# Optimization experiments

Hardware: AMD Instinct MI355X
Metric: run time of the kernel (lower is better)

Reference implementation:

```python
import jax, jax.numpy as jnp
import numpy as np

H = 16      # query heads
KV = 8      # kv heads
D = 128     # head_dim
HID = 2048  # hidden_size
T = 2048    # tokens
EPS = 1e-6
THETA = 1000000.0


def setup_inputs() -> dict:
    key = jax.random.key(0)
    ks = jax.random.split(key, 4)
    return {
        "hidden_states": jax.random.normal(ks[0], (T, HID), jnp.float32),
        "positions": jnp.arange(T, dtype=jnp.int32),
        "qkv_w": jax.random.normal(ks[1], (H * D + 2 * KV * D, HID), jnp.float32) * 0.02,
        "o_w": jax.random.normal(ks[2], (HID, H * D), jnp.float32) * 0.02,
        "q_norm_w": jnp.ones((D,), jnp.float32),
        "k_norm_w": jnp.ones((D,), jnp.float32),
    }


def _rmsnorm(x, w):
    # x: [T, heads, D]; normalize over last dim
    var = jnp.mean(x * x, axis=-1, keepdims=True)
    return x * jax.lax.rsqrt(var + EPS) * w


def _rope(x, positions):
    # neox-style rotate-half; x: [T, heads, D]
    half = D // 2
    inv_freq = 1.0 / (THETA ** (jnp.arange(0, half, dtype=jnp.float32) / half * 1.0))
    inv_freq = 1.0 / (THETA ** (jnp.arange(0, D, 2, dtype=jnp.float32) / D))
    ang = positions.astype(jnp.float32)[:, None] * inv_freq  # [T, D/2]
    cos = jnp.cos(ang)[:, None, :]
    sin = jnp.sin(ang)[:, None, :]
    x1, x2 = x[..., :half], x[..., half:]
    return jnp.concatenate([x1 * cos - x2 * sin, x2 * cos + x1 * sin], axis=-1)


def reference(hidden_states, positions, qkv_w, o_w, q_norm_w, k_norm_w):
    scale = D ** -0.5
    qkv = hidden_states @ qkv_w.T  # [T, H*D + 2*KV*D]
    q = qkv[:, : H * D].reshape(T, H, D)
    k = qkv[:, H * D : H * D + KV * D].reshape(T, KV, D)
    v = qkv[:, H * D + KV * D :].reshape(T, KV, D)

    q = _rope(_rmsnorm(q, q_norm_w), positions)
    k = _rope(_rmsnorm(k, k_norm_w), positions)

    # GQA: repeat kv heads to match query heads
    rep = H // KV
    k = jnp.repeat(k, rep, axis=1)  # [T, H, D]
    v = jnp.repeat(v, rep, axis=1)

    scores = jnp.einsum("thd,shd->hts", q, k) * scale  # [H, T, T]
    causal = positions[:, None] >= positions[None, :]  # [T, T]
    scores = jnp.where(causal[None, :, :], scores, jnp.float32(-1e30))
    p = jax.nn.softmax(scores, axis=-1)
    o = jnp.einsum("hts,shd->thd", p, v).reshape(T, H * D)
    return o @ o_w.T  # [T, HID]
```

## Files before the change

kernel.cpp:

```cpp
#include <hip/hip_runtime.h>
#include <math.h>

#define T_TOK 2048
#define HID 2048
#define NH 16
#define NKV 8
#define HD 128
#define QKV_N 4096
#define EPS 1e-6f

typedef unsigned short u16;
typedef unsigned int   u32;
typedef __attribute__((ext_vector_type(8))) u16   u16x8;
typedef __attribute__((ext_vector_type(8))) short short8;
typedef __attribute__((ext_vector_type(4))) float floatx4;
typedef __attribute__((ext_vector_type(16))) float f32x16;
typedef __attribute__((ext_vector_type(4))) u32   u32x4;

__device__ __forceinline__ u16 f2bf(float x) {
    u32 u = __float_as_uint(x);
    u = (u + 0x7fffu + ((u >> 16) & 1u)) >> 16;
    return (u16)u;
}
__device__ __forceinline__ float bf2f(u16 h) {
    return __uint_as_float(((u32)h) << 16);
}
__device__ __forceinline__ u32 cvtpk_bf16(float lo, float hi) {
    u32 r;
    asm("v_cvt_pk_bf16_f32 %0, %1, %2" : "=v"(r) : "v"(lo), "v"(hi));
    return r;
}

__device__ __forceinline__ void cvt8(const float* __restrict__ in,
                                     u16* __restrict__ out, size_t i)
{
    float4 a = *(const float4*)(in + i);
    float4 b = *(const float4*)(in + i + 4);
    u16x8 o;
    o[0] = f2bf(a.x); o[1] = f2bf(a.y); o[2] = f2bf(a.z); o[3] = f2bf(a.w);
    o[4] = f2bf(b.x); o[5] = f2bf(b.y); o[6] = f2bf(b.z); o[7] = f2bf(b.w);
    *(u16x8*)(out + i) = o;
}

__global__ __launch_bounds__(256) void cvt_pair(
    const float* __restrict__ ina, u16* __restrict__ outa,
    const float* __restrict__ inb, u16* __restrict__ outb)
{
    const int bid = blockIdx.x;
    if (bid < 2048) cvt8(ina, outa, ((size_t)bid * 256 + threadIdx.x) * 8);
    else            cvt8(inb, outb, ((size_t)(bid - 2048) * 256 + threadIdx.x) * 8);
}

#define GBM 256
#define GBN 128
#define GBK 64
#define BUFSH 24576

#define WAITV6 asm volatile("s_waitcnt vmcnt(6)" ::: "memory")
#define WAITV0 asm volatile("s_waitcnt vmcnt(0)" ::: "memory")
#define LGKM0  asm volatile("s_waitcnt lgkmcnt(0)" ::: "memory")
#define BARR   asm volatile("s_barrier" ::: "memory")
#define SB     __builtin_amdgcn_sched_barrier(0)

#define STAGEU(i, tt, dstb) \
    __builtin_amdgcn_global_load_lds( \
        (const __attribute__((address_space(1))) u32*)(gsrc[i] + (size_t)(tt)*GBK), \
        (__attribute__((address_space(3))) u32*)((dstb) + loff[i]), 16, 0, 0)

#define RD_A(dst, srcb, f) do { \
    dst[0] = *(const short8*)((srcb) + arow + (f)*1024 + achunk0); \
    dst[1] = *(const short8*)((srcb) + arow + (f)*1024 + achunk1); } while (0)

#define RD_B(dst, srcb) do { \
    _Pragma("unroll") \
    for (int j_ = 0; j_ < 4; ++j_) { \
        dst[j_][0] = *(const short8*)((srcb) + 16384 + brow + j_*1024 + achunk0); \
        dst[j_][1] = *(const short8*)((srcb) + 16384 + brow + j_*1024 + achunk1); } } while (0)

#define MM(f, aa, bb) do { \
    __builtin_amdgcn_s_setprio(1); \
    _Pragma("unroll") \
    for (int j_ = 0; j_ < 4; ++j_) { \
        acc[f][j_] = __builtin_amdgcn_mfma_f32_16x16x32_bf16(aa[0], bb[j_][0], acc[f][j_], 0, 0, 0); \
        acc[f][j_] = __builtin_amdgcn_mfma_f32_16x16x32_bf16(aa[1], bb[j_][1], acc[f][j_], 0, 0, 0); } \
    __builtin_amdgcn_s_setprio(0); } while (0)

#define TILE(t, CURB, NXTB, THDB, BBC, BBN) do { \
    const bool st_ = (t) + 2 < nt; \
    if (st_) { STAGEU(0, (t)+2, THDB); STAGEU(1, (t)+2, THDB); } \
    RD_A(aP1, CURB, 1); SB; \
    MM(0, aP0, BBC); SB; \
    if (st_) { STAGEU(2, (t)+2, THDB); STAGEU(3, (t)+2, THDB); } \
    RD_A(aP0, CURB, 2); SB; \
    MM(1, aP1, BBC); SB; \
    if (st_) { STAGEU(4, (t)+2, THDB); STAGEU(5, (t)+2, THDB); } \
    RD_A(aP1, CURB, 3); SB; \
    MM(2, aP0, BBC); \
    if ((t) + 1 < nt) { \
        if (st_) { WAITV6; } else { WAITV0; } \
        LGKM0; BARR; SB; \
        RD_B(BBN, NXTB); RD_A(aP0, NXTB, 0); \
    } \
    SB; \
    MM(3, aP1, BBC); SB; \
} while (0)

template<bool OUT_BF16>
__global__ __launch_bounds__(512, 2) void gemm_bt_8p(
    const u16* __restrict__ A, const u16* __restrict__ B,
    void* __restrict__ Cv, int K, int lda, int ldb, int ldc)
{
    extern __shared__ short lds[];
    const int tid = threadIdx.x;
    const int w  = tid >> 6;
    const int l  = tid & 63;
    const int m0 = blockIdx.y * GBM;
    const int n0 = blockIdx.x * GBN;
    const int mr = (w >> 1) * 64;
    const int nc = (w & 1) * 64;
    const int cc = l & 15;
    const int q4 = l >> 4;

    const int lr = l >> 3;
    const int gchunk = ((l & 7) ^ (lr & 7)) * 8;
    const u16* gsrc[6]; int loff[6];
    #pragma unroll
    for (int i = 0; i < 6; ++i) {
        const int u = w * 6 + i;
        if (u < 32) {
            gsrc[i] = A + (size_t)(m0 + u*8 + lr) * lda + gchunk;
            loff[i] = u * 512;
        } else {
            const int v = u - 32;
            gsrc[i] = B + (size_t)(n0 + v*8 + lr) * ldb + gchunk;
            loff[i] = 16384 + v * 512;
        }
    }

    const int achunk0 = ((q4)     ^ (cc & 7)) * 8;
    const int achunk1 = ((4 + q4) ^ (cc & 7)) * 8;
    const int arow = (mr + cc) * 64;
    const int brow = (nc + cc) * 64;

    floatx4 acc[4][4];
    #pragma unroll
    for (int f = 0; f < 4; ++f)
        #pragma unroll
        for (int j = 0; j < 4; ++j) acc[f][j] = (floatx4){0.f, 0.f, 0.f, 0.f};

    short8 aP0[2], aP1[2], bbE[4][2], bbO[4][2];
    short* b0 = lds;
    short* b1 = lds + BUFSH;
    short* b2 = lds + 2 * BUFSH;
    const int nt = K >> 6;

    #pragma unroll
    for (int i = 0; i < 6; ++i) STAGEU(i, 0, b0);
    #pragma unroll
    for (int i = 0; i < 6; ++i) STAGEU(i, 1, b1);
    WAITV6; BARR; SB;
    RD_B(bbE, b0); RD_A(aP0, b0, 0);

    short *CURB = b0, *NXTB = b1, *THDB = b2;
    for (int t = 0; t < nt; t += 2) {
        TILE(t, CURB, NXTB, THDB, bbE, bbO);
        { short* tmp = CURB; CURB = NXTB; NXTB = THDB; THDB = tmp; }
        TILE(t + 1, CURB, NXTB, THDB, bbO, bbE);
        { short* tmp = CURB; CURB = NXTB; NXTB = THDB; THDB = tmp; }
    }

    const int r0 = q4 * 4;
    #pragma unroll
    for (int f = 0; f < 4; ++f)
        #pragma unroll
        for (int j = 0; j < 4; ++j)
            #pragma unroll
            for (int r = 0; r < 4; ++r) {
                const int row = m0 + mr + f*16 + r0 + r;
                const int col = n0 + nc + j*16 + cc;
                if (OUT_BF16)
                    ((u16*)Cv)[(size_t)row * ldc + col] = f2bf(acc[f][j][r]);
                else
                    ((float*)Cv)[(size_t)row * ldc + col] = acc[f][j][r];
            }
}

__global__ __launch_bounds__(256) void prep(
    u16* __restrict__ qkv, const int* __restrict__ positions,
    const float* __restrict__ qw, const float* __restrict__ kw,
    u16* __restrict__ Kp, u16* __restrict__ Vtp)
{
    const int bid = blockIdx.x;
    const int tile = bid & 31, kvh = bid >> 5;
    const int tid = threadIdx.x;
    const int w = tid >> 6, l = tid & 63;
    const int t0 = tile * 64;

    const float qw0 = qw[2*l], qw1 = qw[2*l+1];
    const float kw0 = kw[2*l], kw1 = kw[2*l+1];
    const int   i0  = (2*l) & 63;
    const float if0 = exp2f(-(float)i0     * 0.311430758895690f);
    const float if1 = exp2f(-(float)(i0+1) * 0.311430758895690f);

    for (int rr = w; rr < 64; rr += 4) {
        const int t = t0 + rr;
        const int pos = positions[t];
        const float a0 = (float)pos * if0;
        const float a1 = (float)pos * if1;
        const float s0 = sinf(a0), c0 = cosf(a0);
        const float s1 = sinf(a1), c1 = cosf(a1);

        #pragma unroll
        for (int pass = 0; pass < 3; ++pass) {
            const int off = (pass < 2) ? (2*kvh + pass)*HD : NH*HD + kvh*HD;
            const float w0 = (pass < 2) ? qw0 : kw0;
            const float w1 = (pass < 2) ? qw1 : kw1;
            u16* p = qkv + (size_t)t*QKV_N + off;

            const u32 pk = *(const u32*)(p + 2*l);
            const float x0 = bf2f((u16)pk), x1 = bf2f((u16)(pk >> 16));
            float ss = x0*x0 + x1*x1;
            #pragma unroll
            for (int x = 1; x < 64; x <<= 1) ss += __shfl_xor(ss, x);
            const float rs = rsqrtf(ss * (1.0f/128.0f) + EPS);
            const float xn0 = x0 * rs * w0, xn1 = x1 * rs * w1;
            const float px0 = __shfl_xor(xn0, 32);
            const float px1 = __shfl_xor(xn1, 32);

            float o0, o1;
            if (l < 32) { o0 = xn0*c0 - px0*s0; o1 = xn1*c1 - px1*s1; }
            else        { o0 = xn0*c0 + px0*s0; o1 = xn1*c1 + px1*s1; }
            const u32 outpk = (u32)f2bf(o0) | ((u32)f2bf(o1) << 16);

            if (pass < 2) {
                *(u32*)(p + 2*l) = outpk;
            } else {
                const int ch = l >> 2;
                u16* dst = Kp + ((size_t)(kvh*32 + tile)*64 + rr)*128
                              + (ch ^ (rr & 15))*8 + (l & 3)*2;
                *(u32*)dst = outpk;
            }
        }
    }

    __shared__ u16 tl[64][136];
    {
        const int t  = tid >> 2;
        const int c0 = (tid & 3) * 32;
        const u16* src = qkv + (size_t)(t0 + t)*QKV_N + NH*HD + NKV*HD + kvh*HD + c0;
        #pragma unroll
        for (int p2 = 0; p2 < 4; ++p2)
            *(u16x8*)(&tl[t][c0 + p2*8]) = *(const u16x8*)(src + p2*8);
    }
    __syncthreads();
    {
        u16* dstb = Vtp + (size_t)(kvh*32 + tile) * 128 * 64;
        #pragma unroll
        for (int i = 0; i < 4; ++i) {
            const int id = tid*4 + i;
            const int d = id >> 3;
            const int o = id & 7;
            const int sb = (o ^ (d & 7)) * 8;
            u16x8 v;
            #pragma unroll
            for (int j = 0; j < 8; ++j) v[j] = tl[sb + j][d];
            *(u16x8*)(dstb + d*64 + o*8) = v;
        }
    }
}

__global__ __launch_bounds__(256, 2) void attn_mfma32(
    const u16* __restrict__ qkv, const u16* __restrict__ Kp,
    const u16* __restrict__ Vtp,
    u16* __restrict__ P0, u16* __restrict__ P1,
    u16* __restrict__ P2, u16* __restrict__ P3,
    float2* __restrict__ ml)
{
    const int id   = blockIdx.x;
    const int kvh  = id & 7;
    const int u    = id >> 3;
    const int b5   = u >> 5;
    const int r5   = u & 31;
    const int hp   = r5 & 1;
    const int part = (r5 >> 1) & 3;
    const int q3   = r5 >> 3;
    const int qt   = b5 ? 7 - q3 : q3;
    const int h    = kvh*2 + hp;
    const int t0q  = qt * 256;

    const int tid = threadIdx.x;
    const int w   = tid >> 6;
    const int l   = tid & 63;
    const int q31 = l & 31;
    const int hi  = l >> 5;

    __shared__ short Ks[2][8192];
    __shared__ short Vts[2][8192];

    short8 qf[2][8];
    #pragma unroll
    for (int qg = 0; qg < 2; ++qg) {
        const u16* qrow = qkv + (size_t)(t0q + w*64 + qg*32 + q31) * QKV_N + h*HD;
        #pragma unroll
        for (int ks = 0; ks < 8; ++ks)
            qf[qg][ks] = *(const short8*)(qrow + ks*16 + hi*8);
    }

    float m_run[2] = {-3.0e38f, -3.0e38f}, l_run[2] = {0.f, 0.f};
    f32x16 accO[2][4];
    #pragma unroll
    for (int qg = 0; qg < 2; ++qg)
        #pragma unroll
        for (int nd = 0; nd < 4; ++nd)
            #pragma unroll
            for (int r = 0; r < 16; ++r) accO[qg][nd][r] = 0.f;

    const float Cs = 0.12751744f;

    const int tlo = part * (qt + 1);
    const int thi = tlo + (qt + 1);

    auto issue = [&](int tile, int buf) {
        const size_t tb = (size_t)(kvh*32 + tile) * 8192;
        const u16* g = ((w < 2) ? Kp : Vtp) + tb + (w & 1)*4096 + l*8;
        short* p = ((w < 2) ? Ks[buf] : Vts[buf]) + (w & 1)*4096 + l*8;
        #pragma unroll
        for (int i = 0; i < 8; ++i)
            __builtin_amdgcn_global_load_lds(
                (const __attribute__((address_space(1))) u32*)(g + i*512),
                (__attribute__((address_space(3))) u32*)(p + i*512), 16, 0, 0);
    };

    issue(tlo, 0);
    int cur = 0;

    for (int tt = tlo; tt < thi; ++tt) {
        __syncthreads();
        if (tt + 1 < thi) issue(tt + 1, cur ^ 1);

        const short* Kc = Ks[cur];
        const short* Vc = Vts[cur];

        #pragma unroll
        for (int sub = 0; sub < 2; ++sub) {
            f32x16 accS[2];
            #pragma unroll
            for (int r = 0; r < 16; ++r) { accS[0][r] = 0.f; accS[1][r] = 0.f; }

            __builtin_amdgcn_s_setprio(1);
            #pragma unroll
            for (int ks = 0; ks < 8; ++ks) {
                short8 a = *(const short8*)(Kc + (sub*32 + q31)*128
                                            + ((2*ks + hi) ^ (q31 & 15))*8);
                accS[0] = __builtin_amdgcn_mfma_f32_32x32x16_bf16(a, qf[0][ks], accS[0], 0, 0, 0);
                accS[1] = __builtin_amdgcn_mfma_f32_32x32x16_bf16(a, qf[1][ks], accS[1], 0, 0, 0);
            }
            __builtin_amdgcn_s_setprio(0);

            if (tt >= 4*qt) {
                const int kvb0 = tt*64 + sub*32 + (hi<<2);
                #pragma unroll
                for (int qg = 0; qg < 2; ++qg) {
                    const int qg_g = t0q + w*64 + qg*32 + q31;
                    #pragma unroll
                    for (int r = 0; r < 16; ++r) {
                        const int kvg = kvb0 + (r&3) + 8*(r>>2);
                        if (kvg > qg_g) accS[qg][r] = -1.0e30f;
                    }
                }
            }

            #pragma unroll
            for (int qg = 0; qg < 2; ++qg) {
                float mx = accS[qg][0];
                #pragma unroll
                for (int r = 1; r < 16; ++r) mx = fmaxf(mx, accS[qg][r]);
                mx = fmaxf(mx, __shfl_xor(mx, 32));

                if (__any(mx > m_run[qg] + 11.76f)) {
                    const float m_new = fmaxf(m_run[qg], mx);
                    const float alpha = exp2f((m_run[qg] - m_new) * Cs);
                    l_run[qg] *= alpha;
                    m_run[qg] = m_new;
                    #pragma unroll
                    for (int r = 0; r < 16; ++r) {
                        const float ar = __shfl(alpha, ((r&3) + 8*(r>>2)) + (hi<<2));
                        accO[qg][0][r] *= ar; accO[qg][1][r] *= ar;
                        accO[qg][2][r] *= ar; accO[qg][3][r] *= ar;
                    }
                }
                const float mb = m_run[qg] * Cs;
                float lsum = 0.f;
                #pragma unroll
                for (int r = 0; r < 16; ++r) {
                    const float e = exp2f(accS[qg][r]*Cs - mb);
                    accS[qg][r] = e;
                    lsum += e;
                }
                lsum += __shfl_xor(lsum, 32);
                l_run[qg] += lsum;
            }

            __builtin_amdgcn_s_setprio(1);
            #pragma unroll
            for (int ks2 = 0; ks2 < 2; ++ks2) {
                const int R = ks2 * 8;
                short8 aP[2];
                #pragma unroll
                for (int qg = 0; qg < 2; ++qg) {
                    u32 x0 = cvtpk_bf16(accS[qg][R+0], accS[qg][R+1]);
                    u32 x1 = cvtpk_bf16(accS[qg][R+2], accS[qg][R+3]);
                    u32 x2 = cvtpk_bf16(accS[qg][R+4], accS[qg][R+5]);
                    u32 x3 = cvtpk_bf16(accS[qg][R+6], accS[qg][R+7]);
                    asm("v_permlane32_swap_b32 %0, %1" : "+v"(x0), "+v"(x2));
                    asm("v_permlane32_swap_b32 %0, %1" : "+v"(x1), "+v"(x3));
                    u32x4 aw; aw.x = x0; aw.y = x1; aw.z = x2; aw.w = x3;
                    aP[qg] = __builtin_bit_cast(short8, aw);
                }
                const int ksg = sub*2 + ks2;
                #pragma unroll
                for (int nd = 0; nd < 4; ++nd) {
                    short8 bv = *(const short8*)(Vc + (nd*32 + q31)*64
                                                 + ((2*ksg + hi) ^ (q31 & 7))*8);
                    accO[0][nd] = __builtin_amdgcn_mfma_f32_32x32x16_bf16(aP[0], bv, accO[0][nd], 0, 0, 0);
                    accO[1][nd] = __builtin_amdgcn_mfma_f32_32x32x16_bf16(aP[1], bv, accO[1][nd], 0, 0, 0);
                }
            }
            __builtin_amdgcn_s_setprio(0);
        }
        cur ^= 1;
    }

    u16* Op = (part == 0) ? P0 : (part == 1) ? P1 : (part == 2) ? P2 : P3;
    const size_t hb = (size_t)h * T_TOK;
    #pragma unroll
    for (int qg = 0; qg < 2; ++qg) {
        #pragma unroll
        for (int r = 0; r < 16; ++r) {
            const int qr = (r&3) + 8*(r>>2) + (hi<<2);
            u16* op = Op + (hb + t0q + w*64 + qg*32 + qr) * HD;
            op[q31]      = f2bf(accO[qg][0][r]);
            op[32 + q31] = f2bf(accO[qg][1][r]);
            op[64 + q31] = f2bf(accO[qg][2][r]);
            op[96 + q31] = f2bf(accO[qg][3][r]);
        }
        if (l < 32)
            ml[(size_t)part*NH*T_TOK + hb + t0q + w*64 + qg*32 + l]
                = make_float2(m_run[qg], l_run[qg]);
    }
}

__global__ __launch_bounds__(256) void combine4_cvt(
    const u16* __restrict__ P0, const u16* __restrict__ P1,
    const u16* __restrict__ P2, const u16* __restrict__ P3,
    const float2* __restrict__ ml, u16* __restrict__ qkv,
    const float* __restrict__ ow, u16* __restrict__ owbf)
{
    const int bid = blockIdx.x;
    if (bid >= 2048) {
        cvt8(ow, owbf, ((size_t)(bid - 2048) * 256 + threadIdx.x) * 8);
        return;
    }
    const int idx = bid * 256 + threadIdx.x;
    const int c16 = idx & 15;
    const int t   = (idx >> 4) & (T_TOK - 1);
    const int h   = idx >> 15;
    const size_t base = (size_t)h * T_TOK + t;
    const size_t NT = (size_t)NH * T_TOK;
    const float2 a = ml[base];
    const float2 b = ml[base + NT];
    const float2 c = ml[base + 2*NT];
    const float2 d = ml[base + 3*NT];
    const float Cs = 0.12751744f;
    const float mM = fmaxf(fmaxf(a.x, b.x), fmaxf(c.x, d.x));
    const float wA = exp2f((a.x - mM) * Cs);
    const float wB = exp2f((b.x - mM) * Cs);
    const float wC = exp2f((c.x - mM) * Cs);
    const float wD = exp2f((d.x - mM) * Cs);
    const float inv = 1.0f / (wA*a.y + wB*b.y + wC*c.y + wD*d.y);
    const u16x8 A = *(const u16x8*)(P0 + base * HD + c16*8);
    const u16x8 B = *(const u16x8*)(P1 + base * HD + c16*8);
    const u16x8 C = *(const u16x8*)(P2 + base * HD + c16*8);
    const u16x8 D = *(const u16x8*)(P3 + base * HD + c16*8);
    u16x8 o;
    #pragma unroll
    for (int j = 0; j < 8; ++j)
        o[j] = f2bf((wA*bf2f(A[j]) + wB*bf2f(B[j]) + wC*bf2f(C[j]) + wD*bf2f(D[j])) * inv);
    *(u16x8*)(qkv + (size_t)t * QKV_N + h * HD + c16*8) = o;
}

extern "C" void kernel_launch(void* const* d_in, const int* in_sizes, int n_in,
                              void* d_out, int out_size, void* d_ws, size_t ws_size,
                              hipStream_t stream)
{
    const float* hidden    = (const float*)d_in[0];
    const int*   positions = (const int*)  d_in[1];
    const float* qkv_w     = (const float*)d_in[2];
    const float* o_w       = (const float*)d_in[3];
    const float* q_norm_w  = (const float*)d_in[4];
    const float* k_norm_w  = (const float*)d_in[5];
    float* out = (float*)d_out;

    u16* qkvbf = (u16*)d_ws;
    u16* wbf   = qkvbf + (size_t)T_TOK * QKV_N;
    u16* abf   = wbf   + (size_t)QKV_N * HID;
    u16* kpb   = abf   + (size_t)T_TOK * HID;
    u16* vpb   = kpb   + (size_t)NKV * T_TOK * HD;

    u16* P0 = wbf;
    u16* P1 = wbf + (size_t)NH * T_TOK * HD;
    u16* P2 = abf;
    u16* P3 = (u16*)out;
    float2* mlp = (float2*)((u16*)out + (size_t)NH * T_TOK * HD);

    static bool s_attr = false;
    if (!s_attr) {
        (void)hipFuncSetAttribute(
            reinterpret_cast<const void*>(&gemm_bt_8p<true>),
            hipFuncAttributeMaxDynamicSharedMemorySize, 147456);
        (void)hipFuncSetAttribute(
            reinterpret_cast<const void*>(&gemm_bt_8p<false>),
            hipFuncAttributeMaxDynamicSharedMemorySize, 147456);
        s_attr = true;
    }

    cvt_pair<<<6144, 256, 0, stream>>>(hidden, abf, qkv_w, wbf);

    gemm_bt_8p<true><<<dim3(QKV_N/GBN, T_TOK/GBM), 512, 147456, stream>>>(
        abf, wbf, qkvbf, HID, HID, HID, QKV_N);

    prep<<<256, 256, 0, stream>>>(qkvbf, positions, q_norm_w, k_norm_w, kpb, vpb);

    attn_mfma32<<<512, 256, 0, stream>>>(qkvbf, kpb, vpb, P0, P1, P2, P3, mlp);

    combine4_cvt<<<4096, 256, 0, stream>>>(P0, P1, P2, P3, mlp, qkvbf, o_w, kpb);

    gemm_bt_8p<false><<<dim3(HID/GBN, T_TOK/GBM), 512, 147456, stream>>>(
        qkvbf, kpb, out, HID, QKV_N, HID, HID);
}
```

Before: 268.6 us.

## Halve attention query and KV tiles, double grid and occupancy

The attention kernel now works on 128-row query tiles (32 rows per wave) and 32-token KV tiles instead of 256/64. The grid doubles to 1024 blocks and launch bounds allow 4 blocks per CU. The V-transpose layout in prep and the LDS swizzle change to match 32-token tiles. This aims to improve occupancy and load balance across the causal work. In exchange, each K/V tile loaded into LDS is reused by fewer query rows, and there are twice as many barriers per unit of work.

```diff
diff --git a/kernel.cpp b/kernel.cpp
--- a/kernel.cpp
+++ b/kernel.cpp
@@ -254,22 +254,21 @@
     }
     __syncthreads();
     {
-        u16* dstb = Vtp + (size_t)(kvh*32 + tile) * 128 * 64;
+        u16* dstb = Vtp + (size_t)(kvh*64 + tile*2) * 4096;
         #pragma unroll
         for (int i = 0; i < 4; ++i) {
             const int id = tid*4 + i;
             const int d = id >> 3;
             const int o = id & 7;
-            const int sb = (o ^ (d & 7)) * 8;
             u16x8 v;
             #pragma unroll
-            for (int j = 0; j < 8; ++j) v[j] = tl[sb + j][d];
-            *(u16x8*)(dstb + d*64 + o*8) = v;
-        }
-    }
-}
-
-__global__ __launch_bounds__(256, 2) void attn_mfma32(
+            for (int j = 0; j < 8; ++j) v[j] = tl[o*8 + j][d];
+            *(u16x8*)(dstb + (o >> 2)*4096 + d*32 + (((o & 3) ^ (d & 3)))*8) = v;
+        }
+    }
+}
+
+__global__ __launch_bounds__(256, 4) void attn_mfma32(
     const u16* __restrict__ qkv, const u16* __restrict__ Kp,
     const u16* __restrict__ Vtp,
     u16* __restrict__ P0, u16* __restrict__ P1,
@@ -279,14 +278,14 @@
     const int id   = blockIdx.x;
     const int kvh  = id & 7;
     const int u    = id >> 3;
-    const int b5   = u >> 5;
-    const int r5   = u & 31;
-    const int hp   = r5 & 1;
-    const int part = (r5 >> 1) & 3;
-    const int q3   = r5 >> 3;
-    const int qt   = b5 ? 7 - q3 : q3;
+    const int hp   = u & 1;
+    const int part = (u >> 1) & 3;
+    const int q4b  = u >> 3;
+    const int g    = q4b & 3;
+    const int s4   = q4b >> 2;
+    const int qt   = (s4 & 1) ? (2*g + (s4 >> 1)) : ((15 - (s4 >> 1)) - 2*g);
     const int h    = kvh*2 + hp;
-    const int t0q  = qt * 256;
+    const int t0q  = qt * 128;
 
     const int tid = threadIdx.x;
     const int w   = tid >> 6;
@@ -294,40 +293,37 @@
     const int q31 = l & 31;
     const int hi  = l >> 5;
 
-    __shared__ short Ks[2][8192];
-    __shared__ short Vts[2][8192];
-
-    short8 qf[2][8];
-    #pragma unroll
-    for (int qg = 0; qg < 2; ++qg) {
-        const u16* qrow = qkv + (size_t)(t0q + w*64 + qg*32 + q31) * QKV_N + h*HD;
+    __shared__ short Ks[2][4096];
+    __shared__ short Vts[2][4096];
+
+    short8 qf[8];
+    {
+        const u16* qrow = qkv + (size_t)(t0q + w*32 + q31) * QKV_N + h*HD;
         #pragma unroll
         for (int ks = 0; ks < 8; ++ks)
-            qf[qg][ks] = *(const short8*)(qrow + ks*16 + hi*8);
-    }
-
-    float m_run[2] = {-3.0e38f, -3.0e38f}, l_run[2] = {0.f, 0.f};
-    f32x16 accO[2][4];
-    #pragma unroll
-    for (int qg = 0; qg < 2; ++qg)
-        #pragma unroll
-        for (int nd = 0; nd < 4; ++nd)
-            #pragma unroll
-            for (int r = 0; r < 16; ++r) accO[qg][nd][r] = 0.f;
+            qf[ks] = *(const short8*)(qrow + ks*16 + hi*8);
+    }
+
+    float m_run = -3.0e38f, l_run = 0.f;
+    f32x16 accO[4];
+    #pragma unroll
+    for (int nd = 0; nd < 4; ++nd)
+        #pragma unroll
+        for (int r = 0; r < 16; ++r) accO[nd][r] = 0.f;
 
     const float Cs = 0.12751744f;
 
     const int tlo = part * (qt + 1);
     const int thi = tlo + (qt + 1);
 
-    auto issue = [&](int tile, int buf) {
-        const size_t tb = (size_t)(kvh*32 + tile) * 8192;
-        const u16* g = ((w < 2) ? Kp : Vtp) + tb + (w & 1)*4096 + l*8;
-        short* p = ((w < 2) ? Ks[buf] : Vts[buf]) + (w & 1)*4096 + l*8;
-        #pragma unroll
-        for (int i = 0; i < 8; ++i)
+    auto issue = [&](int t32, int buf) {
+        const size_t tb = (size_t)(kvh*64 + t32) * 4096;
+        const u16* g2 = ((w < 2) ? Kp : Vtp) + tb + (w & 1)*2048 + l*8;
+        short* p = ((w < 2) ? Ks[buf] : Vts[buf]) + (w & 1)*2048 + l*8;
+        #pragma unroll
+        for (int i = 0; i < 4; ++i)
             __builtin_amdgcn_global_load_lds(
-                (const __attribute__((address_space(1))) u32*)(g + i*512),
+                (const __attribute__((address_space(1))) u32*)(g2 + i*512),
                 (__attribute__((address_space(3))) u32*)(p + i*512), 16, 0, 0);
     };
 
@@ -341,113 +337,99 @@
         const short* Kc = Ks[cur];
         const short* Vc = Vts[cur];
 
-        #pragma unroll
-        for (int sub = 0; sub < 2; ++sub) {
-            f32x16 accS[2];
+        f32x16 accS;
+        #pragma unroll
+        for (int r = 0; r < 16; ++r) accS[r] = 0.f;
+
+        __builtin_amdgcn_s_setprio(1);
+        #pragma unroll
+        for (int ks = 0; ks < 8; ++ks) {
+            short8 a = *(const short8*)(Kc + q31*128 + ((2*ks + hi) ^ (q31 & 15))*8);
+            accS = __builtin_amdgcn_mfma_f32_32x32x16_bf16(a, qf[ks], accS, 0, 0, 0);
+        }
+        __builtin_amdgcn_s_setprio(0);
+
+        if (tt >= 4*qt) {
+            const int kvb0 = tt*32 + (hi << 2);
+            const int qg_g = t0q + w*32 + q31;
             #pragma unroll
-            for (int r = 0; r < 16; ++r) { accS[0][r] = 0.f; accS[1][r] = 0.f; }
-
-            __builtin_amdgcn_s_setprio(1);
+            for (int r = 0; r < 16; ++r) {
+                const int kvg = kvb0 + (r&3) + 8*(r>>2);
+                if (kvg > qg_g) accS[r] = -1.0e30f;
+            }
+        }
+
+        float mx = accS[0];
+        #pragma unroll
+        for (int r = 1; r < 16; ++r) mx = fmaxf(mx, accS[r]);
+        mx = fmaxf(mx, __shfl_xor(mx, 32));
+
+        if (__any(mx > m_run + 11.76f)) {
+            const float m_new = fmaxf(m_run, mx);
+            const float alpha = exp2f((m_run - m_new) * Cs);
+            l_run *= alpha;
+            m_run = m_new;
             #pragma unroll
-            for (int ks = 0; ks < 8; ++ks) {
-                short8 a = *(const short8*)(Kc + (sub*32 + q31)*128
-                                            + ((2*ks + hi) ^ (q31 & 15))*8);
-                accS[0] = __builtin_amdgcn_mfma_f32_32x32x16_bf16(a, qf[0][ks], accS[0], 0, 0, 0);
-                accS[1] = __builtin_amdgcn_mfma_f32_32x32x16_bf16(a, qf[1][ks], accS[1], 0, 0, 0);
+            for (int r = 0; r < 16; ++r) {
+                const float ar = __shfl(alpha, ((r&3) + 8*(r>>2)) + (hi<<2));
+                accO[0][r] *= ar; accO[1][r] *= ar;
+                accO[2][r] *= ar; accO[3][r] *= ar;
             }
-            __builtin_amdgcn_s_setprio(0);
-
-            if (tt >= 4*qt) {
-                const int kvb0 = tt*64 + sub*32 + (hi<<2);
-                #pragma unroll
-                for (int qg = 0; qg < 2; ++qg) {
-                    const int qg_g = t0q + w*64 + qg*32 + q31;
-                    #pragma unroll
-                    for (int r = 0; r < 16; ++r) {
-                        const int kvg = kvb0 + (r&3) + 8*(r>>2);
-                        if (kvg > qg_g) accS[qg][r] = -1.0e30f;
-                    }
-                }
+        }
+        const float mb = m_run * Cs;
+        float lsum = 0.f;
+        #pragma unroll
+        for (int r = 0; r < 16; ++r) {
+            const float e = exp2f(accS[r]*Cs - mb);
+            accS[r] = e;
+            lsum += e;
+        }
+        lsum += __shfl_xor(lsum, 32);
+        l_run += lsum;
+
+        short8 aP[2];
+        #pragma unroll
+        for (int ks2 = 0; ks2 < 2; ++ks2) {
+            const int R = ks2 * 8;
+            u32 x0 = cvtpk_bf16(accS[R+0], accS[R+1]);
+            u32 x1 = cvtpk_bf16(accS[R+2], accS[R+3]);
+            u32 x2 = cvtpk_bf16(accS[R+4], accS[R+5]);
+            u32 x3 = cvtpk_bf16(accS[R+6], accS[R+7]);
+            asm("v_permlane32_swap_b32 %0, %1" : "+v"(x0), "+v"(x2));
+            asm("v_permlane32_swap_b32 %0, %1" : "+v"(x1), "+v"(x3));
+            u32x4 aw; aw.x = x0; aw.y = x1; aw.z = x2; aw.w = x3;
+            aP[ks2] = __builtin_bit_cast(short8, aw);
+        }
+
+        __builtin_amdgcn_s_setprio(1);
+        #pragma unroll
+        for (int ks2 = 0; ks2 < 2; ++ks2) {
+            #pragma unroll
+            for (int nd = 0; nd < 4; ++nd) {
+                short8 bv = *(const short8*)(Vc + (nd*32 + q31)*32
+                                             + ((ks2*2 + hi) ^ (q31 & 3))*8);
+                accO[nd] = __builtin_amdgcn_mfma_f32_32x32x16_bf16(aP[ks2], bv, accO[nd], 0, 0, 0);
             }
-
-            #pragma unroll
-            for (int qg = 0; qg < 2; ++qg) {
-                float mx = accS[qg][0];
-                #pragma unroll
-                for (int r = 1; r < 16; ++r) mx = fmaxf(mx, accS[qg][r]);
-                mx = fmaxf(mx, __shfl_xor(mx, 32));
-
-                if (__any(mx > m_run[qg] + 11.76f)) {
-                    const float m_new = fmaxf(m_run[qg], mx);
-                    const float alpha = exp2f((m_run[qg] - m_new) * Cs);
-                    l_run[qg] *= alpha;
-                    m_run[qg] = m_new;
-                    #pragma unroll
-                    for (int r = 0; r < 16; ++r) {
-                        const float ar = __shfl(alpha, ((r&3) + 8*(r>>2)) + (hi<<2));
-                        accO[qg][0][r] *= ar; accO[qg][1][r] *= ar;
-                        accO[qg][2][r] *= ar; accO[qg][3][r] *= ar;
-                    }
-                }
-                const float mb = m_run[qg] * Cs;
-                float lsum = 0.f;
-                #pragma unroll
-                for (int r = 0; r < 16; ++r) {
-                    const float e = exp2f(accS[qg][r]*Cs - mb);
-                    accS[qg][r] = e;
-                    lsum += e;
-                }
-                lsum += __shfl_xor(lsum, 32);
-                l_run[qg] += lsum;
-            }
-
-            __builtin_amdgcn_s_setprio(1);
-            #pragma unroll
-            for (int ks2 = 0; ks2 < 2; ++ks2) {
-                const int R = ks2 * 8;
-                short8 aP[2];
-                #pragma unroll
-                for (int qg = 0; qg < 2; ++qg) {
-                    u32 x0 = cvtpk_bf16(accS[qg][R+0], accS[qg][R+1]);
-                    u32 x1 = cvtpk_bf16(accS[qg][R+2], accS[qg][R+3]);
-                    u32 x2 = cvtpk_bf16(accS[qg][R+4], accS[qg][R+5]);
-                    u32 x3 = cvtpk_bf16(accS[qg][R+6], accS[qg][R+7]);
-                    asm("v_permlane32_swap_b32 %0, %1" : "+v"(x0), "+v"(x2));
-                    asm("v_permlane32_swap_b32 %0, %1" : "+v"(x1), "+v"(x3));
-                    u32x4 aw; aw.x = x0; aw.y = x1; aw.z = x2; aw.w = x3;
-                    aP[qg] = __builtin_bit_cast(short8, aw);
-                }
-                const int ksg = sub*2 + ks2;
-                #pragma unroll
-                for (int nd = 0; nd < 4; ++nd) {
-                    short8 bv = *(const short8*)(Vc + (nd*32 + q31)*64
-                                                 + ((2*ksg + hi) ^ (q31 & 7))*8);
-                    accO[0][nd] = __builtin_amdgcn_mfma_f32_32x32x16_bf16(aP[0], bv, accO[0][nd], 0, 0, 0);
-                    accO[1][nd] = __builtin_amdgcn_mfma_f32_32x32x16_bf16(aP[1], bv, accO[1][nd], 0, 0, 0);
-                }
-            }
-            __builtin_amdgcn_s_setprio(0);
-        }
+        }
+        __builtin_amdgcn_s_setprio(0);
+
         cur ^= 1;
     }
 
     u16* Op = (part == 0) ? P0 : (part == 1) ? P1 : (part == 2) ? P2 : P3;
     const size_t hb = (size_t)h * T_TOK;
     #pragma unroll
-    for (int qg = 0; qg < 2; ++qg) {
-        #pragma unroll
-        for (int r = 0; r < 16; ++r) {
-            const int qr = (r&3) + 8*(r>>2) + (hi<<2);
-            u16* op = Op + (hb + t0q + w*64 + qg*32 + qr) * HD;
-            op[q31]      = f2bf(accO[qg][0][r]);
-            op[32 + q31] = f2bf(accO[qg][1][r]);
-            op[64 + q31] = f2bf(accO[qg][2][r]);
-            op[96 + q31] = f2bf(accO[qg][3][r]);
-        }
-        if (l < 32)
-            ml[(size_t)part*NH*T_TOK + hb + t0q + w*64 + qg*32 + l]
-                = make_float2(m_run[qg], l_run[qg]);
-    }
+    for (int r = 0; r < 16; ++r) {
+        const int qr = (r&3) + 8*(r>>2) + (hi<<2);
+        u16* op = Op + (hb + t0q + w*32 + qr) * HD;
+        op[q31]      = f2bf(accO[0][r]);
+        op[32 + q31] = f2bf(accO[1][r]);
+        op[64 + q31] = f2bf(accO[2][r]);
+        op[96 + q31] = f2bf(accO[3][r]);
+    }
+    if (l < 32)
+        ml[(size_t)part*NH*T_TOK + hb + t0q + w*32 + l]
+            = make_float2(m_run, l_run);
 }
 
 __global__ __launch_bounds__(256) void combine4_cvt(
@@ -531,7 +513,7 @@
 
     prep<<<256, 256, 0, stream>>>(qkvbf, positions, q_norm_w, k_norm_w, kpb, vpb);
 
-    attn_mfma32<<<512, 256, 0, stream>>>(qkvbf, kpb, vpb, P0, P1, P2, P3, mlp);
+    attn_mfma32<<<1024, 256, 0, stream>>>(qkvbf, kpb, vpb, P0, P1, P2, P3, mlp);
 
     combine4_cvt<<<4096, 256, 0, stream>>>(P0, P1, P2, P3, mlp, qkvbf, o_w, kpb);
 
```

Result: no change. 272.0 us (+1.3%).

## Split-K the output projection and rebalance attention blocks across both heads of a KV group

Applied to the files above, without the earlier changes.

The output projection GEMM gets a split-K mode: a grid z-dimension of 2 gives each half of K its own block and partial output, and a new elementwise kernel adds the two fp32 partials. This doubles the number of blocks for the small 2048x2048 GEMM, which otherwise launches only 128 blocks, to raise CU occupancy, at the cost of an extra read/write pass over the output. Separately, the attention kernel now gives each block 128 query rows for both query heads sharing one KV head, instead of 256 rows for one head. KV tiles are split evenly over the 4 partitions, and the causal mask is shared across both heads. This reuses each loaded K/V tile for two heads and balances causal work, with slight changes to setprio placement.

```diff
diff --git a/kernel.cpp b/kernel.cpp
--- a/kernel.cpp
+++ b/kernel.cpp
@@ -49,6 +49,20 @@
     const int bid = blockIdx.x;
     if (bid < 2048) cvt8(ina, outa, ((size_t)bid * 256 + threadIdx.x) * 8);
     else            cvt8(inb, outb, ((size_t)(bid - 2048) * 256 + threadIdx.x) * 8);
+}
+
+__global__ __launch_bounds__(256) void addf32(
+    float* __restrict__ out, const float* __restrict__ part)
+{
+    const size_t i = ((size_t)blockIdx.x * 256 + threadIdx.x) * 8;
+    float4 a0 = *(const float4*)(out + i);
+    float4 a1 = *(const float4*)(out + i + 4);
+    float4 b0 = *(const float4*)(part + i);
+    float4 b1 = *(const float4*)(part + i + 4);
+    a0.x += b0.x; a0.y += b0.y; a0.z += b0.z; a0.w += b0.w;
+    a1.x += b1.x; a1.y += b1.y; a1.z += b1.z; a1.w += b1.w;
+    *(float4*)(out + i)     = a0;
+    *(float4*)(out + i + 4) = a1;
 }
 
 #define GBM 256
@@ -108,7 +122,8 @@
 template<bool OUT_BF16>
 __global__ __launch_bounds__(512, 2) void gemm_bt_8p(
     const u16* __restrict__ A, const u16* __restrict__ B,
-    void* __restrict__ Cv, int K, int lda, int ldb, int ldc)
+    void* __restrict__ Cv, void* __restrict__ Cv2,
+    int Ks, int lda, int ldb, int ldc)
 {
     extern __shared__ short lds[];
     const int tid = threadIdx.x;
@@ -116,6 +131,10 @@
     const int l  = tid & 63;
     const int m0 = blockIdx.y * GBM;
     const int n0 = blockIdx.x * GBN;
+    const int z  = blockIdx.z;
+    A += (size_t)z * Ks;
+    B += (size_t)z * Ks;
+    void* Cw = z ? Cv2 : Cv;
     const int mr = (w >> 1) * 64;
     const int nc = (w & 1) * 64;
     const int cc = l & 15;
@@ -152,7 +171,7 @@
     short* b0 = lds;
     short* b1 = lds + BUFSH;
     short* b2 = lds + 2 * BUFSH;
-    const int nt = K >> 6;
+    const int nt = Ks >> 6;
 
     #pragma unroll
     for (int i = 0; i < 6; ++i) STAGEU(i, 0, b0);
@@ -179,9 +198,9 @@
                 const int row = m0 + mr + f*16 + r0 + r;
                 const int col = n0 + nc + j*16 + cc;
                 if (OUT_BF16)
-                    ((u16*)Cv)[(size_t)row * ldc + col] = f2bf(acc[f][j][r]);
+                    ((u16*)Cw)[(size_t)row * ldc + col] = f2bf(acc[f][j][r]);
                 else
-                    ((float*)Cv)[(size_t)row * ldc + col] = acc[f][j][r];
+                    ((float*)Cw)[(size_t)row * ldc + col] = acc[f][j][r];
             }
 }
 
@@ -276,17 +295,13 @@
     u16* __restrict__ P2, u16* __restrict__ P3,
     float2* __restrict__ ml)
 {
-    const int id   = blockIdx.x;
-    const int kvh  = id & 7;
-    const int u    = id >> 3;
-    const int b5   = u >> 5;
-    const int r5   = u & 31;
-    const int hp   = r5 & 1;
-    const int part = (r5 >> 1) & 3;
-    const int q3   = r5 >> 3;
-    const int qt   = b5 ? 7 - q3 : q3;
-    const int h    = kvh*2 + hp;
-    const int t0q  = qt * 256;
+    const int id  = blockIdx.x;
+    const int kvh = id & 7;
+    const int u   = id >> 3;
+    const int p   = u & 3;
+    const int uq  = u >> 2;
+    const int qt  = (uq < 8) ? uq : 23 - uq;
+    const int t0q = qt * 128;
 
     const int tid = threadIdx.x;
     const int w   = tid >> 6;
@@ -299,44 +314,48 @@
 
     short8 qf[2][8];
     #pragma unroll
-    for (int qg = 0; qg < 2; ++qg) {
-        const u16* qrow = qkv + (size_t)(t0q + w*64 + qg*32 + q31) * QKV_N + h*HD;
+    for (int h2 = 0; h2 < 2; ++h2) {
+        const u16* qrow = qkv + (size_t)(t0q + w*32 + q31) * QKV_N
+                              + (kvh*2 + h2)*HD;
         #pragma unroll
         for (int ks = 0; ks < 8; ++ks)
-            qf[qg][ks] = *(const short8*)(qrow + ks*16 + hi*8);
+            qf[h2][ks] = *(const short8*)(qrow + ks*16 + hi*8);
     }
 
     float m_run[2] = {-3.0e38f, -3.0e38f}, l_run[2] = {0.f, 0.f};
     f32x16 accO[2][4];
     #pragma unroll
-    for (int qg = 0; qg < 2; ++qg)
+    for (int h2 = 0; h2 < 2; ++h2)
         #pragma unroll
         for (int nd = 0; nd < 4; ++nd)
             #pragma unroll
-            for (int r = 0; r < 16; ++r) accO[qg][nd][r] = 0.f;
+            for (int r = 0; r < 16; ++r) accO[h2][nd][r] = 0.f;
 
     const float Cs = 0.12751744f;
 
-    const int tlo = part * (qt + 1);
-    const int thi = tlo + (qt + 1);
+    const int nt   = 2*qt + 2;
+    const int base = nt >> 2;
+    const int rem  = nt & 3;
+    const int tlo  = p*base + (p < rem ? p : rem);
+    const int thi  = tlo + base + (p < rem ? 1 : 0);
 
     auto issue = [&](int tile, int buf) {
         const size_t tb = (size_t)(kvh*32 + tile) * 8192;
         const u16* g = ((w < 2) ? Kp : Vtp) + tb + (w & 1)*4096 + l*8;
-        short* p = ((w < 2) ? Ks[buf] : Vts[buf]) + (w & 1)*4096 + l*8;
+        short* pl = ((w < 2) ? Ks[buf] : Vts[buf]) + (w & 1)*4096 + l*8;
         #pragma unroll
         for (int i = 0; i < 8; ++i)
             __builtin_amdgcn_global_load_lds(
                 (const __attribute__((address_space(1))) u32*)(g + i*512),
-                (__attribute__((address_space(3))) u32*)(p + i*512), 16, 0, 0);
+                (__attribute__((address_space(3))) u32*)(pl + i*512), 16, 0, 0);
     };
 
-    issue(tlo, 0);
+    if (tlo < thi) issue(tlo, 0);
     int cur = 0;
 
-    for (int tt = tlo; tt < thi; ++tt) {
+    for (int tile = tlo; tile < thi; ++tile) {
         __syncthreads();
-        if (tt + 1 < thi) issue(tt + 1, cur ^ 1);
+        if (tile + 1 < thi) issue(tile + 1, cur ^ 1);
 
         const short* Kc = Ks[cur];
         const short* Vc = Vts[cur];
@@ -357,67 +376,64 @@
             }
             __builtin_amdgcn_s_setprio(0);
 
-            if (tt >= 4*qt) {
-                const int kvb0 = tt*64 + sub*32 + (hi<<2);
+            if (tile >= 2*qt) {
+                const int kvb0 = tile*64 + sub*32 + (hi << 2);
+                const int qg   = t0q + w*32 + q31;
                 #pragma unroll
-                for (int qg = 0; qg < 2; ++qg) {
-                    const int qg_g = t0q + w*64 + qg*32 + q31;
-                    #pragma unroll
-                    for (int r = 0; r < 16; ++r) {
-                        const int kvg = kvb0 + (r&3) + 8*(r>>2);
-                        if (kvg > qg_g) accS[qg][r] = -1.0e30f;
-                    }
+                for (int r = 0; r < 16; ++r) {
+                    const int kvg = kvb0 + (r&3) + 8*(r>>2);
+                    if (kvg > qg) { accS[0][r] = -1.0e30f; accS[1][r] = -1.0e30f; }
                 }
             }
 
             #pragma unroll
-            for (int qg = 0; qg < 2; ++qg) {
-                float mx = accS[qg][0];
+            for (int h2 = 0; h2 < 2; ++h2) {
+                float mx = accS[h2][0];
                 #pragma unroll
-                for (int r = 1; r < 16; ++r) mx = fmaxf(mx, accS[qg][r]);
+                for (int r = 1; r < 16; ++r) mx = fmaxf(mx, accS[h2][r]);
                 mx = fmaxf(mx, __shfl_xor(mx, 32));
 
-                if (__any(mx > m_run[qg] + 11.76f)) {
-                    const float m_new = fmaxf(m_run[qg], mx);
-                    const float alpha = exp2f((m_run[qg] - m_new) * Cs);
-                    l_run[qg] *= alpha;
-                    m_run[qg] = m_new;
+                if (__any(mx > m_run[h2] + 11.76f)) {
+                    const float m_new = fmaxf(m_run[h2], mx);
+                    const float alpha = exp2f((m_run[h2] - m_new) * Cs);
+                    l_run[h2] *= alpha;
+                    m_run[h2] = m_new;
                     #pragma unroll
                     for (int r = 0; r < 16; ++r) {
                         const float ar = __shfl(alpha, ((r&3) + 8*(r>>2)) + (hi<<2));
-                        accO[qg][0][r] *= ar; accO[qg][1][r] *= ar;
-                        accO[qg][2][r] *= ar; accO[qg][3][r] *= ar;
+                        accO[h2][0][r] *= ar; accO[h2][1][r] *= ar;
+                        accO[h2][2][r] *= ar; accO[h2][3][r] *= ar;
                     }
                 }
-                const float mb = m_run[qg] * Cs;
+                const float mb = m_run[h2] * Cs;
                 float lsum = 0.f;
                 #pragma unroll
                 for (int r = 0; r < 16; ++r) {
-                    const float e = exp2f(accS[qg][r]*Cs - mb);
-                    accS[qg][r] = e;
+                    const float e = exp2f(accS[h2][r]*Cs - mb);
+                    accS[h2][r] = e;
                     lsum += e;
                 }
                 lsum += __shfl_xor(lsum, 32);
-                l_run[qg] += lsum;
+                l_run[h2] += lsum;
             }
 
-            __builtin_amdgcn_s_setprio(1);
             #pragma unroll
             for (int ks2 = 0; ks2 < 2; ++ks2) {
                 const int R = ks2 * 8;
                 short8 aP[2];
                 #pragma unroll
-                for (int qg = 0; qg < 2; ++qg) {
-                    u32 x0 = cvtpk_bf16(accS[qg][R+0], accS[qg][R+1]);
-                    u32 x1 = cvtpk_bf16(accS[qg][R+2], accS[qg][R+3]);
-                    u32 x2 = cvtpk_bf16(accS[qg][R+4], accS[qg][R+5]);
-                    u32 x3 = cvtpk_bf16(accS[qg][R+6], accS[qg][R+7]);
+                for (int h2 = 0; h2 < 2; ++h2) {
+                    u32 x0 = cvtpk_bf16(accS[h2][R+0], accS[h2][R+1]);
+                    u32 x1 = cvtpk_bf16(accS[h2][R+2], accS[h2][R+3]);
+                    u32 x2 = cvtpk_bf16(accS[h2][R+4], accS[h2][R+5]);
+                    u32 x3 = cvtpk_bf16(accS[h2][R+6], accS[h2][R+7]);
                     asm("v_permlane32_swap_b32 %0, %1" : "+v"(x0), "+v"(x2));
                     asm("v_permlane32_swap_b32 %0, %1" : "+v"(x1), "+v"(x3));
                     u32x4 aw; aw.x = x0; aw.y = x1; aw.z = x2; aw.w = x3;
-                    aP[qg] = __builtin_bit_cast(short8, aw);
+                    aP[h2] = __builtin_bit_cast(short8, aw);
                 }
                 const int ksg = sub*2 + ks2;
+                __builtin_amdgcn_s_setprio(1);
                 #pragma unroll
                 for (int nd = 0; nd < 4; ++nd) {
                     short8 bv = *(const short8*)(Vc + (nd*32 + q31)*64
@@ -425,28 +441,28 @@
                     accO[0][nd] = __builtin_amdgcn_mfma_f32_32x32x16_bf16(aP[0], bv, accO[0][nd], 0, 0, 0);
                     accO[1][nd] = __builtin_amdgcn_mfma_f32_32x32x16_bf16(aP[1], bv, accO[1][nd], 0, 0, 0);
                 }
+                __builtin_amdgcn_s_setprio(0);
             }
-            __builtin_amdgcn_s_setprio(0);
         }
         cur ^= 1;
     }
 
-    u16* Op = (part == 0) ? P0 : (part == 1) ? P1 : (part == 2) ? P2 : P3;
-    const size_t hb = (size_t)h * T_TOK;
-    #pragma unroll
-    for (int qg = 0; qg < 2; ++qg) {
+    u16* Op = (p == 0) ? P0 : (p == 1) ? P1 : (p == 2) ? P2 : P3;
+    #pragma unroll
+    for (int h2 = 0; h2 < 2; ++h2) {
+        const size_t hb = (size_t)(kvh*2 + h2) * T_TOK;
         #pragma unroll
         for (int r = 0; r < 16; ++r) {
             const int qr = (r&3) + 8*(r>>2) + (hi<<2);
-            u16* op = Op + (hb + t0q + w*64 + qg*32 + qr) * HD;
-            op[q31]      = f2bf(accO[qg][0][r]);
-            op[32 + q31] = f2bf(accO[qg][1][r]);
-            op[64 + q31] = f2bf(accO[qg][2][r]);
-            op[96 + q31] = f2bf(accO[qg][3][r]);
+            u16* op = Op + (hb + t0q + w*32 + qr) * HD;
+            op[q31]      = f2bf(accO[h2][0][r]);
+            op[32 + q31] = f2bf(accO[h2][1][r]);
+            op[64 + q31] = f2bf(accO[h2][2][r]);
+            op[96 + q31] = f2bf(accO[h2][3][r]);
         }
         if (l < 32)
-            ml[(size_t)part*NH*T_TOK + hb + t0q + w*64 + qg*32 + l]
-                = make_float2(m_run[qg], l_run[qg]);
+            ml[(size_t)p*NH*T_TOK + hb + t0q + w*32 + l]
+                = make_float2(m_run[h2], l_run[h2]);
     }
 }
 
@@ -512,6 +528,7 @@
     u16* P2 = abf;
     u16* P3 = (u16*)out;
     float2* mlp = (float2*)((u16*)out + (size_t)NH * T_TOK * HD);
+    float* partC = (float*)wbf;
 
     static bool s_attr = false;
     if (!s_attr) {
@@ -526,8 +543,8 @@
 
     cvt_pair<<<6144, 256, 0, stream>>>(hidden, abf, qkv_w, wbf);
 
-    gemm_bt_8p<true><<<dim3(QKV_N/GBN, T_TOK/GBM), 512, 147456, stream>>>(
-        abf, wbf, qkvbf, HID, HID, HID, QKV_N);
+    gemm_bt_8p<true><<<dim3(QKV_N/GBN, T_TOK/GBM, 1), 512, 147456, stream>>>(
+        abf, wbf, qkvbf, qkvbf, HID, HID, HID, QKV_N);
 
     prep<<<256, 256, 0, stream>>>(qkvbf, positions, q_norm_w, k_norm_w, kpb, vpb);
 
@@ -535,6 +552,8 @@
 
     combine4_cvt<<<4096, 256, 0, stream>>>(P0, P1, P2, P3, mlp, qkvbf, o_w, kpb);
 
-    gemm_bt_8p<false><<<dim3(HID/GBN, T_TOK/GBM), 512, 147456, stream>>>(
-        qkvbf, kpb, out, HID, QKV_N, HID, HID);
-}
+    gemm_bt_8p<false><<<dim3(HID/GBN, T_TOK/GBM, 2), 512, 147456, stream>>>(
+        qkvbf, kpb, out, partC, HID/2, QKV_N, HID, HID);
+
+    addf32<<<(T_TOK*HID)/2048, 256, 0, stream>>>(out, partC);
+}
```

Result: slower. 276.1 us (+2.8%).
